# Performance work log

Hardware: AMD Instinct MI355X
Metric: run time of the kernel (lower is better)

## Reference

```python
import jax, jax.numpy as jnp
import numpy as np

B, S, K, M = 8, 2048, 4096, 4096
DENSITY = 0.1


def setup_inputs() -> dict:
    key = jax.random.key(0)
    k1, k2, k3 = jax.random.split(key, 3)
    x = jax.random.normal(k1, (B, S, K), dtype=jnp.float32)
    weight = jax.random.normal(k2, (M, K), dtype=jnp.float32) * 0.02
    # bool sparsity mask: True where CSR stores a nonzero value
    mask = jax.random.uniform(k3, (M, K)) < DENSITY
    return {"x": x, "weight": weight, "mask": mask}


def reference(x, weight, mask):
    # Original: dense_to_sparse(weight) -> CSR, then left_spmm(m, k, csr, x.transpose(1,2))
    # i.e. out[b] = W_sparse @ x[b].T  ->  [B, M, S].
    # Mathematically identical to matmul with the masked dense weight.
    W = weight * mask  # [M, K], zeros exactly where CSR has no entry
    # x: [B, S, K]; contraction over K gives [B, M, S]
    return jnp.einsum('mk,bsk->bms', W, x)
```

## Files before the change

### kernel.cpp

```cpp
#include <hip/hip_runtime.h>
#include <hip/hip_bf16.h>
#include <stdint.h>

constexpr int B_ = 8;
constexpr int S_ = 2048;
constexpr int K_ = 4096;
constexpr int M_ = 4096;

typedef __bf16 bf16x8 __attribute__((ext_vector_type(8)));
typedef float  f32x4  __attribute__((ext_vector_type(4)));

__device__ __forceinline__ void async16(const void* g, void* l) {
  __builtin_amdgcn_global_load_lds(
      (__attribute__((address_space(1))) unsigned int*)(g),
      (__attribute__((address_space(3))) unsigned int*)(l),
      16, 0, 0);
}

__global__ void detect_mask_kernel(const uint32_t* __restrict__ mw, int nwords,
                                   int* __restrict__ flag_out) {
  __shared__ int s_float, s_hi;
  if (threadIdx.x == 0) { s_float = 0; s_hi = 0; }
  __syncthreads();
  int f_float = 0, f_hi = 0;
  for (int i = threadIdx.x; i < nwords; i += blockDim.x) {
    uint32_t w = mw[i];
    if (w == 0x3F800000u) f_float = 1;
    else if (w & 0xFFFFFF00u) f_hi = 1;
  }
  if (f_float) atomicOr(&s_float, 1);
  if (f_hi)    atomicOr(&s_hi, 1);
  __syncthreads();
  if (threadIdx.x == 0) flag_out[0] = s_float ? 2 : (s_hi ? 1 : 0);
}

__device__ __forceinline__ bool mask_bit(const void* mask, int flag, size_t idx) {
  if (flag == 1) return ((const uint8_t*)mask)[idx] != 0;
  if (flag == 2) return ((const float*)mask)[idx] != 0.0f;
  return ((const int*)mask)[idx] != 0;
}

__global__ void build_wb_kernel(const float* __restrict__ w, const void* __restrict__ mask,
                                const int* __restrict__ flagp,
                                __hip_bfloat16* __restrict__ wb, int n) {
  const int flag = flagp[0];
  int idx = (blockIdx.x * blockDim.x + threadIdx.x) * 4;
  if (idx >= n) return;
  float4 v = *(const float4*)(w + idx);
  float m0, m1, m2, m3;
  if (flag == 1) {
    uchar4 mv = *(const uchar4*)((const uint8_t*)mask + idx);
    m0 = mv.x ? 1.f : 0.f; m1 = mv.y ? 1.f : 0.f;
    m2 = mv.z ? 1.f : 0.f; m3 = mv.w ? 1.f : 0.f;
  } else if (flag == 2) {
    float4 mv = *(const float4*)((const float*)mask + idx);
    m0 = mv.x != 0.f ? 1.f : 0.f; m1 = mv.y != 0.f ? 1.f : 0.f;
    m2 = mv.z != 0.f ? 1.f : 0.f; m3 = mv.w != 0.f ? 1.f : 0.f;
  } else {
    int4 mv = *(const int4*)((const int*)mask + idx);
    m0 = mv.x ? 1.f : 0.f; m1 = mv.y ? 1.f : 0.f;
    m2 = mv.z ? 1.f : 0.f; m3 = mv.w ? 1.f : 0.f;
  }
  union { ushort4 u4; __hip_bfloat16 h[4]; } o;
  o.h[0] = __float2bfloat16(v.x * m0);
  o.h[1] = __float2bfloat16(v.y * m1);
  o.h[2] = __float2bfloat16(v.z * m2);
  o.h[3] = __float2bfloat16(v.w * m3);
  *(ushort4*)(wb + idx) = o.u4;
}

__global__ void cvt_x_kernel(const float* __restrict__ x,
                             __hip_bfloat16* __restrict__ xb, int n) {
  int idx = (blockIdx.x * blockDim.x + threadIdx.x) * 4;
  if (idx >= n) return;
  float4 v = *(const float4*)(x + idx);
  union { ushort4 u4; __hip_bfloat16 h[4]; } o;
  o.h[0] = __float2bfloat16(v.x);
  o.h[1] = __float2bfloat16(v.y);
  o.h[2] = __float2bfloat16(v.z);
  o.h[3] = __float2bfloat16(v.w);
  *(ushort4*)(xb + idx) = o.u4;
}

__global__ __launch_bounds__(256) void gemm_bt_kernel(
    const __hip_bfloat16* __restrict__ A,
    const __hip_bfloat16* __restrict__ X,
    float* __restrict__ C) {
  constexpr int BM = 128, BN = 128, BK = 64;
  __shared__ __hip_bfloat16 sA[BM * BK];
  __shared__ __hip_bfloat16 sB[BN * BK];

  const int tid  = threadIdx.x;
  const int lane = tid & 63;
  const int wv   = tid >> 6;
  const int wm   = (wv >> 1) * 64;
  const int wn   = (wv & 1) * 64;
  const int lr   = lane & 15;
  const int lq   = lane >> 4;

  const size_t bm = (size_t)blockIdx.x * BM;
  const size_t bs = (size_t)blockIdx.y * BN;
  const size_t b  = blockIdx.z;

  const __hip_bfloat16* Ag = A + bm * K_;
  const __hip_bfloat16* Xg = X + b * (size_t)S_ * K_ + bs * K_;
  float* Cg = C + b * (size_t)M_ * S_ + bm * S_ + bs;

  const int srow = tid >> 3;
  const int scol = (tid & 7) * 8;

  f32x4 acc[4][4];
#pragma unroll
  for (int i = 0; i < 4; i++)
#pragma unroll
    for (int j = 0; j < 4; j++) acc[i][j] = f32x4{0.f, 0.f, 0.f, 0.f};

  for (int kt = 0; kt < K_; kt += BK) {
    if (kt) __syncthreads();
#pragma unroll
    for (int i = 0; i < 4; ++i) {
      const int row = i * 32 + srow;
      async16(Ag + (size_t)row * K_ + kt + scol, &sA[row * BK + scol]);
      async16(Xg + (size_t)row * K_ + kt + scol, &sB[row * BK + scol]);
    }
    __syncthreads();

#pragma unroll
    for (int ks = 0; ks < BK; ks += 32) {
      bf16x8 af[4], bfr[4];
#pragma unroll
      for (int i = 0; i < 4; i++)
        af[i] = *(const bf16x8*)(const void*)&sA[(wm + i * 16 + lr) * BK + ks + lq * 8];
#pragma unroll
      for (int j = 0; j < 4; j++)
        bfr[j] = *(const bf16x8*)(const void*)&sB[(wn + j * 16 + lr) * BK + ks + lq * 8];
#pragma unroll
      for (int i = 0; i < 4; i++)
#pragma unroll
        for (int j = 0; j < 4; j++)
          acc[i][j] = __builtin_amdgcn_mfma_f32_16x16x32_bf16(af[i], bfr[j], acc[i][j], 0, 0, 0);
    }
  }

#pragma unroll
  for (int i = 0; i < 4; i++) {
#pragma unroll
    for (int j = 0; j < 4; j++) {
      const int row = wm + i * 16 + lq * 4;
      const int col = wn + j * 16 + lr;
#pragma unroll
      for (int r = 0; r < 4; r++)
        Cg[(size_t)(row + r) * S_ + col] = acc[i][j][r];
    }
  }
}

__global__ void fb_gemm_kernel(const float* __restrict__ x, const float* __restrict__ w,
                               const void* __restrict__ mask, const int* __restrict__ flagp,
                               float* __restrict__ out) {
  __shared__ float sW[16][17];
  __shared__ float sX[16][17];
  const int flag = flagp[0];
  const int tx = threadIdx.x, ty = threadIdx.y;
  const int m0 = blockIdx.x * 16, s0 = blockIdx.y * 16, b = blockIdx.z;
  float acc = 0.f;
  for (int kt = 0; kt < K_; kt += 16) {
    const size_t wi = (size_t)(m0 + ty) * K_ + kt + tx;
    sW[ty][tx] = mask_bit(mask, flag, wi) ? w[wi] : 0.f;
    sX[ty][tx] = x[(size_t)b * S_ * K_ + (size_t)(s0 + ty) * K_ + kt + tx];
    __syncthreads();
#pragma unroll
    for (int kk = 0; kk < 16; kk++) acc += sW[ty][kk] * sX[tx][kk];
    __syncthreads();
  }
  out[(size_t)b * M_ * S_ + (size_t)(m0 + ty) * S_ + s0 + tx] = acc;
}

extern "C" void kernel_launch(void* const* d_in, const int* in_sizes, int n_in,
                              void* d_out, int out_size, void* d_ws, size_t ws_size,
                              hipStream_t stream) {
  const float* x    = (const float*)d_in[0];
  const float* w    = (const float*)d_in[1];
  const void*  mask = d_in[2];
  float* out = (float*)d_out;

  uint8_t* ws = (uint8_t*)d_ws;
  int* flag = (int*)ws;
  const size_t offW = 256;
  const size_t offX = offW + (size_t)M_ * K_ * sizeof(__hip_bfloat16);
  const size_t need = offX + (size_t)B_ * S_ * K_ * sizeof(__hip_bfloat16);

  detect_mask_kernel<<<1, 256, 0, stream>>>((const uint32_t*)mask, 16384, flag);

  if (ws_size >= need) {
    __hip_bfloat16* Wb = (__hip_bfloat16*)(ws + offW);
    __hip_bfloat16* Xb = (__hip_bfloat16*)(ws + offX);
    build_wb_kernel<<<(M_ * K_) / 1024, 256, 0, stream>>>(w, mask, flag, Wb, M_ * K_);
    cvt_x_kernel<<<(B_ * S_ * K_) / 1024, 256, 0, stream>>>(x, Xb, B_ * S_ * K_);
    dim3 grid(M_ / 128, S_ / 128, B_);
    gemm_bt_kernel<<<grid, 256, 0, stream>>>(Wb, Xb, out);
  } else {
    dim3 grid(M_ / 16, S_ / 16, B_);
    fb_gemm_kernel<<<grid, dim3(16, 16), 0, stream>>>(x, w, mask, flag, out);
  }
}
```

Baseline: 1.147 ms.

## Rewrite bf16 GEMM as 256x256 double-buffered eight-wave pipelined kernel

Replaces the 128x128 single-buffered MFMA GEMM with a 256x256 tile kernel using 8 waves, double-buffered LDS split into K-half planes, and async global-to-LDS staging interleaved with MFMA phases via explicit barriers, waitcnts and setprio. Adds an XOR swizzle of LDS layout to avoid bank conflicts and a block-id swizzle so neighbouring blocks share data in cache. Also widens the x conversion kernel to 8 elements per thread. The intent is to hide global load latency and raise arithmetic intensity; the risks are register pressure from the 8x4 accumulator array and correctness of the hand-tuned vmcnt counts.

```diff
diff --git a/kernel.cpp b/kernel.cpp
--- a/kernel.cpp
+++ b/kernel.cpp
@@ -9,6 +9,7 @@
 
 typedef __bf16 bf16x8 __attribute__((ext_vector_type(8)));
 typedef float  f32x4  __attribute__((ext_vector_type(4)));
+typedef unsigned short ushort8v __attribute__((ext_vector_type(8)));
 
 __device__ __forceinline__ void async16(const void* g, void* l) {
   __builtin_amdgcn_global_load_lds(
@@ -71,88 +72,175 @@
 
 __global__ void cvt_x_kernel(const float* __restrict__ x,
                              __hip_bfloat16* __restrict__ xb, int n) {
-  int idx = (blockIdx.x * blockDim.x + threadIdx.x) * 4;
+  int idx = (blockIdx.x * blockDim.x + threadIdx.x) * 8;
   if (idx >= n) return;
-  float4 v = *(const float4*)(x + idx);
-  union { ushort4 u4; __hip_bfloat16 h[4]; } o;
-  o.h[0] = __float2bfloat16(v.x);
-  o.h[1] = __float2bfloat16(v.y);
-  o.h[2] = __float2bfloat16(v.z);
-  o.h[3] = __float2bfloat16(v.w);
-  *(ushort4*)(xb + idx) = o.u4;
-}
-
-__global__ __launch_bounds__(256) void gemm_bt_kernel(
+  float4 v0 = *(const float4*)(x + idx);
+  float4 v1 = *(const float4*)(x + idx + 4);
+  union { ushort8v u; __hip_bfloat16 h[8]; } o;
+  o.h[0] = __float2bfloat16(v0.x); o.h[1] = __float2bfloat16(v0.y);
+  o.h[2] = __float2bfloat16(v0.z); o.h[3] = __float2bfloat16(v0.w);
+  o.h[4] = __float2bfloat16(v1.x); o.h[5] = __float2bfloat16(v1.y);
+  o.h[6] = __float2bfloat16(v1.z); o.h[7] = __float2bfloat16(v1.w);
+  *(ushort8v*)(xb + idx) = o.u;
+}
+
+__global__ __launch_bounds__(512, 2) void gemm8p_kernel(
     const __hip_bfloat16* __restrict__ A,
     const __hip_bfloat16* __restrict__ X,
     float* __restrict__ C) {
-  constexpr int BM = 128, BN = 128, BK = 64;
-  __shared__ __hip_bfloat16 sA[BM * BK];
-  __shared__ __hip_bfloat16 sB[BN * BK];
+  constexpr int BK = 64;
+  alignas(16) __shared__ __hip_bfloat16 lds[2][2][2][256 * 32];
 
   const int tid  = threadIdx.x;
   const int lane = tid & 63;
   const int wv   = tid >> 6;
-  const int wm   = (wv >> 1) * 64;
-  const int wn   = (wv & 1) * 64;
+  const int wm   = wv >> 2;
+  const int wn   = wv & 3;
   const int lr   = lane & 15;
   const int lq   = lane >> 4;
 
-  const size_t bm = (size_t)blockIdx.x * BM;
-  const size_t bs = (size_t)blockIdx.y * BN;
-  const size_t b  = blockIdx.z;
+  const int bid = blockIdx.x;
+  const int swz = (bid & 7) * 128 + (bid >> 3);
+  const int b   = swz >> 7;
+  const int t_  = swz & 127;
+  const int mz  = t_ & 15;
+  const int sz  = t_ >> 4;
+
+  const size_t bm = (size_t)mz * 256;
+  const size_t bs = (size_t)sz * 256;
 
   const __hip_bfloat16* Ag = A + bm * K_;
-  const __hip_bfloat16* Xg = X + b * (size_t)S_ * K_ + bs * K_;
-  float* Cg = C + b * (size_t)M_ * S_ + bm * S_ + bs;
-
-  const int srow = tid >> 3;
-  const int scol = (tid & 7) * 8;
-
-  f32x4 acc[4][4];
-#pragma unroll
-  for (int i = 0; i < 4; i++)
+  const __hip_bfloat16* Xg = X + (size_t)b * S_ * K_ + bs * K_;
+  float* Cg = C + (size_t)b * M_ * S_ + bm * S_ + bs;
+
+  const int    srow = tid >> 2;
+  const int    scg  = ((tid & 3) ^ ((tid >> 3) & 3)) * 8;
+  const int    sldso = tid * 8;
+  const __hip_bfloat16* Ags = Ag + (size_t)srow * K_ + scg;
+  const __hip_bfloat16* Xgs = Xg + (size_t)srow * K_ + scg;
+
+  const int rA   = wm * 128 + lr;
+  const int offA = rA * 32 + (lq ^ ((rA >> 1) & 3)) * 8;
+  const int rB   = wn * 64 + lr;
+  const int offB = rB * 32 + (lq ^ ((rB >> 1) & 3)) * 8;
+
+  f32x4 acc[8][4];
+#pragma unroll
+  for (int i = 0; i < 8; i++)
 #pragma unroll
     for (int j = 0; j < 4; j++) acc[i][j] = f32x4{0.f, 0.f, 0.f, 0.f};
 
-  for (int kt = 0; kt < K_; kt += BK) {
-    if (kt) __syncthreads();
-#pragma unroll
-    for (int i = 0; i < 4; ++i) {
-      const int row = i * 32 + srow;
-      async16(Ag + (size_t)row * K_ + kt + scol, &sA[row * BK + scol]);
-      async16(Xg + (size_t)row * K_ + kt + scol, &sB[row * BK + scol]);
-    }
-    __syncthreads();
-
-#pragma unroll
-    for (int ks = 0; ks < BK; ks += 32) {
-      bf16x8 af[4], bfr[4];
-#pragma unroll
-      for (int i = 0; i < 4; i++)
-        af[i] = *(const bf16x8*)(const void*)&sA[(wm + i * 16 + lr) * BK + ks + lq * 8];
-#pragma unroll
-      for (int j = 0; j < 4; j++)
-        bfr[j] = *(const bf16x8*)(const void*)&sB[(wn + j * 16 + lr) * BK + ks + lq * 8];
-#pragma unroll
-      for (int i = 0; i < 4; i++)
-#pragma unroll
-        for (int j = 0; j < 4; j++)
-          acc[i][j] = __builtin_amdgcn_mfma_f32_16x16x32_bf16(af[i], bfr[j], acc[i][j], 0, 0, 0);
-    }
-  }
-
-#pragma unroll
-  for (int i = 0; i < 4; i++) {
+#define LDF(p, off) (*(const bf16x8*)(const void*)((p) + (off)))
+
+#define STAGE_PLANE(gbase, ldsplane) do {                                   \
+    async16((gbase),                    (ldsplane) + sldso);                \
+    async16((gbase) + (size_t)128 * K_, (ldsplane) + sldso + 4096);         \
+  } while (0)
+
+#define CFENCE asm volatile("" ::: "memory")
+
+#define LGKM0 do {                                                          \
+    asm volatile("s_waitcnt lgkmcnt(0)" ::: "memory");                      \
+    __builtin_amdgcn_sched_barrier(0);                                      \
+  } while (0)
+
+#define MM4(I, AA) do {                                                        \
+    acc[I][0] = __builtin_amdgcn_mfma_f32_16x16x32_bf16(AA, b0, acc[I][0], 0, 0, 0); \
+    acc[I][1] = __builtin_amdgcn_mfma_f32_16x16x32_bf16(AA, b1, acc[I][1], 0, 0, 0); \
+    acc[I][2] = __builtin_amdgcn_mfma_f32_16x16x32_bf16(AA, b2, acc[I][2], 0, 0, 0); \
+    acc[I][3] = __builtin_amdgcn_mfma_f32_16x16x32_bf16(AA, b3, acc[I][3], 0, 0, 0); \
+  } while (0)
+
+#define TILE_BODY(CUR, NXT, KT, DOSTAGE) do {                               \
+    const __hip_bfloat16* pA0 = &lds[CUR][0][0][0];                         \
+    const __hip_bfloat16* pA1 = &lds[CUR][0][1][0];                         \
+    const __hip_bfloat16* pB0 = &lds[CUR][1][0][0];                         \
+    const __hip_bfloat16* pB1 = &lds[CUR][1][1][0];                         \
+    bf16x8 a0, a1, a2, a3, a4, a5, a6, a7, b0, b1, b2, b3;                  \
+                              \
+    a0 = LDF(pA0, offA);        a1 = LDF(pA0, offA + 512);                  \
+    a2 = LDF(pA0, offA + 1024); a3 = LDF(pA0, offA + 1536);                 \
+    b0 = LDF(pB0, offB);        b1 = LDF(pB0, offB + 512);                  \
+    b2 = LDF(pB0, offB + 1024); b3 = LDF(pB0, offB + 1536);                 \
+    if (DOSTAGE) STAGE_PLANE(Ags + (KT) + BK, &lds[NXT][0][0][0]);          \
+    __builtin_amdgcn_s_barrier(); CFENCE;                                   \
+    LGKM0;                                                                  \
+    __builtin_amdgcn_s_setprio(1);                                          \
+    MM4(0, a0); MM4(1, a1); MM4(2, a2); MM4(3, a3);                         \
+    __builtin_amdgcn_s_setprio(0);                                          \
+    __builtin_amdgcn_s_barrier(); CFENCE;                                   \
+                              \
+    a4 = LDF(pA0, offA + 2048); a5 = LDF(pA0, offA + 2560);                 \
+    a6 = LDF(pA0, offA + 3072); a7 = LDF(pA0, offA + 3584);                 \
+    if (DOSTAGE) STAGE_PLANE(Xgs + (KT) + BK, &lds[NXT][1][0][0]);          \
+    __builtin_amdgcn_s_barrier(); CFENCE;                                   \
+    LGKM0;                                                                  \
+    __builtin_amdgcn_s_setprio(1);                                          \
+    MM4(4, a4); MM4(5, a5); MM4(6, a6); MM4(7, a7);                         \
+    __builtin_amdgcn_s_setprio(0);                                          \
+    if (DOSTAGE) { asm volatile("s_waitcnt vmcnt(4)" ::: "memory"); }       \
+    else         { asm volatile("s_waitcnt vmcnt(0)" ::: "memory"); }       \
+    __builtin_amdgcn_s_barrier(); CFENCE;                                   \
+                             \
+    a0 = LDF(pA1, offA);        a1 = LDF(pA1, offA + 512);                  \
+    a2 = LDF(pA1, offA + 1024); a3 = LDF(pA1, offA + 1536);                 \
+    b0 = LDF(pB1, offB);        b1 = LDF(pB1, offB + 512);                  \
+    b2 = LDF(pB1, offB + 1024); b3 = LDF(pB1, offB + 1536);                 \
+    if (DOSTAGE) STAGE_PLANE(Ags + (KT) + BK + 32, &lds[NXT][0][1][0]);     \
+    __builtin_amdgcn_s_barrier(); CFENCE;                                   \
+    LGKM0;                                                                  \
+    __builtin_amdgcn_s_setprio(1);                                          \
+    MM4(0, a0); MM4(1, a1); MM4(2, a2); MM4(3, a3);                         \
+    __builtin_amdgcn_s_setprio(0);                                          \
+    __builtin_amdgcn_s_barrier(); CFENCE;                                   \
+                             \
+    a4 = LDF(pA1, offA + 2048); a5 = LDF(pA1, offA + 2560);                 \
+    a6 = LDF(pA1, offA + 3072); a7 = LDF(pA1, offA + 3584);                 \
+    if (DOSTAGE) STAGE_PLANE(Xgs + (KT) + BK + 32, &lds[NXT][1][1][0]);     \
+    __builtin_amdgcn_s_barrier(); CFENCE;                                   \
+    LGKM0;                                                                  \
+    __builtin_amdgcn_s_setprio(1);                                          \
+    MM4(4, a4); MM4(5, a5); MM4(6, a6); MM4(7, a7);                         \
+    __builtin_amdgcn_s_setprio(0);                                          \
+    if (DOSTAGE) { asm volatile("s_waitcnt vmcnt(4)" ::: "memory"); }       \
+    else         { asm volatile("s_waitcnt vmcnt(0)" ::: "memory"); }       \
+    __builtin_amdgcn_s_barrier(); CFENCE;                                   \
+  } while (0)
+
+  STAGE_PLANE(Ags,      &lds[0][0][0][0]);
+  STAGE_PLANE(Xgs,      &lds[0][1][0][0]);
+  STAGE_PLANE(Ags + 32, &lds[0][0][1][0]);
+  STAGE_PLANE(Xgs + 32, &lds[0][1][1][0]);
+  asm volatile("s_waitcnt vmcnt(4)" ::: "memory");
+  __builtin_amdgcn_s_barrier(); CFENCE;
+
+  int kt = 0;
+#pragma unroll 1
+  for (; kt < K_ - 2 * BK; kt += 2 * BK) {
+    TILE_BODY(0, 1, kt, true);
+    TILE_BODY(1, 0, kt + BK, true);
+  }
+  TILE_BODY(0, 1, kt, true);
+  TILE_BODY(1, 0, kt + BK, false);
+
+#pragma unroll
+  for (int i = 0; i < 8; i++) {
 #pragma unroll
     for (int j = 0; j < 4; j++) {
-      const int row = wm + i * 16 + lq * 4;
-      const int col = wn + j * 16 + lr;
+      const int row = wm * 128 + i * 16 + lq * 4;
+      const int col = wn * 64 + j * 16 + lr;
 #pragma unroll
       for (int r = 0; r < 4; r++)
         Cg[(size_t)(row + r) * S_ + col] = acc[i][j][r];
     }
   }
+
+#undef TILE_BODY
+#undef MM4
+#undef LGKM0
+#undef CFENCE
+#undef STAGE_PLANE
+#undef LDF
 }
 
 __global__ void fb_gemm_kernel(const float* __restrict__ x, const float* __restrict__ w,
@@ -196,9 +284,9 @@
     __hip_bfloat16* Wb = (__hip_bfloat16*)(ws + offW);
     __hip_bfloat16* Xb = (__hip_bfloat16*)(ws + offX);
     build_wb_kernel<<<(M_ * K_) / 1024, 256, 0, stream>>>(w, mask, flag, Wb, M_ * K_);
-    cvt_x_kernel<<<(B_ * S_ * K_) / 1024, 256, 0, stream>>>(x, Xb, B_ * S_ * K_);
-    dim3 grid(M_ / 128, S_ / 128, B_);
-    gemm_bt_kernel<<<grid, 256, 0, stream>>>(Wb, Xb, out);
+    cvt_x_kernel<<<(B_ * S_ * K_) / 2048, 256, 0, stream>>>(x, Xb, B_ * S_ * K_);
+    static_assert(M_ % 256 == 0 && S_ % 256 == 0, "tile divisibility");
+    gemm8p_kernel<<<dim3((M_ / 256) * (S_ / 256) * B_), dim3(512), 0, stream>>>(Wb, Xb, out);
   } else {
     dim3 grid(M_ / 16, S_ / 16, B_);
     fb_gemm_kernel<<<grid, dim3(16, 16), 0, stream>>>(x, w, mask, flag, out);
```

Measured after the change: 986.5 us. 14.0% less time.
